# Performance work log

Hardware: AMD Instinct MI355X
Metric: run time of the kernel (lower is better)

The kernel has to match this reference:

```python
import jax, jax.numpy as jnp
import numpy as np

MOE_TOP_K = 2
MOE_GATE_NORM_STD = 1.0  # moe_gate_norm_std


def setup_inputs() -> dict:
    key = jax.random.key(0)
    k1, k2, k3, k4 = jax.random.split(key, 4)
    T, D, E = 16384, 2048, 8
    return {
        "x": jax.random.normal(k1, (T, D), dtype=jnp.float32),
        "wg_weight": jax.random.normal(k2, (E, D), dtype=jnp.float32) * 0.02,
        "gate_map_weight": jax.random.normal(k3, (E, E), dtype=jnp.float32) * 0.1,
        "gate_residual": jax.random.normal(k4, (T, E), dtype=jnp.float32),
    }


def reference(x, wg_weight, gate_map_weight, gate_residual):
    # Router GEMM in fp32 (module force-casts wg and input to float32)
    logits = jnp.einsum("td,ed->te", x.astype(jnp.float32), wg_weight)  # [T, E]
    # gate_residual path: gate_map Linear(E, E, bias=False)
    logits = logits + jnp.einsum("te,fe->tf", gate_residual, gate_map_weight)

    num_experts = wg_weight.shape[0]
    # gating(): moe_use_mixtral_gating=False, moe_use_logits_norm=True
    # torch.std is unbiased (ddof=1)
    logits_std = jnp.std(logits, axis=1, keepdims=True, ddof=1)
    probs = jax.nn.softmax(logits / (logits_std / MOE_GATE_NORM_STD), axis=1)
    gates, indices = jax.lax.top_k(probs, MOE_TOP_K)  # [T, K]
    # zero out routing to the last expert, then renormalize
    gates = jnp.where(indices == num_experts - 1, jnp.zeros_like(gates), gates)
    gates = gates / jnp.sum(gates, axis=1, keepdims=True)
    # Dense equivalent of the per-expert nonzero-gather dict: (indices, gates)
    # fully determines expert_info[e] = (tokens where indices==e, matching gates).
    return gates, indices, logits
```

## Files before the change

### kernel.cpp

```cpp
#include <hip/hip_runtime.h>
#include <hip/hip_bf16.h>
#include <stdint.h>


#define WAVES_PER_BLOCK 4
#define TOKENS_PER_WAVE 8
#define TOKENS_PER_BLOCK (WAVES_PER_BLOCK * TOKENS_PER_WAVE)
#define DCONST 2048
#define NCHUNK 8

__device__ __forceinline__ unsigned long long shfl_xor_u64(unsigned long long v, int m) {
    int lo = __shfl_xor((int)(uint32_t)v, m, 64);
    int hi = __shfl_xor((int)(uint32_t)(v >> 32), m, 64);
    return ((unsigned long long)(uint32_t)hi << 32) | (unsigned long long)(uint32_t)lo;
}

__global__ __launch_bounds__(256, 2)
void router_kernel(const float* __restrict__ x,
                   const float* __restrict__ wg,
                   const float* __restrict__ gm,
                   const float* __restrict__ gr,
                   float* __restrict__ out,
                   int T)
{
    const int wave = threadIdx.x >> 6;
    const int lane = threadIdx.x & 63;
    const int t0   = blockIdx.x * TOKENS_PER_BLOCK + wave * TOKENS_PER_WAVE;

    __shared__ float swg[8 * DCONST];
    {
        const float4* src = (const float4*)wg;
        float4*       dst = (float4*)swg;
        #pragma unroll
        for (int i = 0; i < 16; ++i)
            dst[threadIdx.x + i * 256] = src[threadIdx.x + i * 256];
    }
    __syncthreads();

    float acc[64];
    #pragma unroll
    for (int v = 0; v < 64; ++v) acc[v] = 0.f;

    const float* xw = x + (size_t)t0 * DCONST + (lane << 2);
    const float* wl = swg + (lane << 2);

    float4 xa[8], xb[8];

    #define LOADX(buf, j)                                                     \
        { _Pragma("unroll")                                                   \
          for (int tt = 0; tt < 8; ++tt)                                      \
              buf[tt] = *(const float4*)(xw + tt * DCONST + (j) * 256); }

    #define COMPUTE(j, buf)                                                   \
        { _Pragma("unroll")                                                   \
          for (int e = 0; e < 8; ++e) {                                       \
              const float4 wf = *(const float4*)(wl + e * DCONST + (j) * 256);\
              _Pragma("unroll")                                               \
              for (int tt = 0; tt < 8; ++tt) {                                \
                  acc[tt * 8 + e] += buf[tt].x * wf.x;                        \
                  acc[tt * 8 + e] += buf[tt].y * wf.y;                        \
                  acc[tt * 8 + e] += buf[tt].z * wf.z;                        \
                  acc[tt * 8 + e] += buf[tt].w * wf.w;                        \
              }                                                               \
          } }

    LOADX(xa, 0);
    #pragma unroll 1
    for (int j = 0; j < NCHUNK - 2; j += 2) {
        LOADX(xb, j + 1);
        COMPUTE(j, xa);
        LOADX(xa, j + 2);
        COMPUTE(j + 1, xb);
    }
    LOADX(xb, NCHUNK - 1);
    COMPUTE(NCHUNK - 2, xa);
    COMPUTE(NCHUNK - 1, xb);

    #pragma unroll
    for (int m = 1; m < 64; m <<= 1) {
        const bool up = (lane & m) != 0;
        #pragma unroll
        for (int v = 0; v < 64; v += 2 * m) {
            const float keep = up ? acc[v + m] : acc[v];
            const float send = up ? acc[v] : acc[v + m];
            const float got  = __shfl_xor(send, m, 64);
            acc[v] = keep + got;
        }
    }
    float logit = acc[0];

    const int tt = lane >> 3;
    const int f  = lane & 7;
    const int t  = t0 + tt;

    const float4 ga = *(const float4*)(gr + (size_t)t * 8);
    const float4 gb = *(const float4*)(gr + (size_t)t * 8 + 4);
    const float4 ma = *(const float4*)(gm + f * 8);
    const float4 mb = *(const float4*)(gm + f * 8 + 4);
    logit += ga.x * ma.x + ga.y * ma.y + ga.z * ma.z + ga.w * ma.w
           + gb.x * mb.x + gb.y * mb.y + gb.z * mb.z + gb.w * mb.w;

    out[(size_t)4 * T + (size_t)t0 * 8 + lane] = logit;

    float s = logit;
    s += __shfl_xor(s, 1, 64);
    s += __shfl_xor(s, 2, 64);
    s += __shfl_xor(s, 4, 64);
    const float mean = s * 0.125f;
    float d2 = (logit - mean) * (logit - mean);
    d2 += __shfl_xor(d2, 1, 64);
    d2 += __shfl_xor(d2, 2, 64);
    d2 += __shfl_xor(d2, 4, 64);
    const float stdv = sqrtf(d2 / 7.0f);

    uint32_t ob = __float_as_uint(logit);
    ob = (ob & 0x80000000u) ? ~ob : (ob | 0x80000000u);
    unsigned long long k1 = ((unsigned long long)ob << 8) | (unsigned long long)(7 - f);
    unsigned long long k2 = 0ull;
    #pragma unroll
    for (int m = 1; m <= 4; m <<= 1) {
        const unsigned long long o1 = shfl_xor_u64(k1, m);
        const unsigned long long o2 = shfl_xor_u64(k2, m);
        const unsigned long long hi = k1 > o1 ? k1 : o1;
        const unsigned long long lo = k1 > o1 ? o1 : k1;
        const unsigned long long so = k2 > o2 ? k2 : o2;
        k1 = hi;
        k2 = lo > so ? lo : so;
    }
    const int i1 = 7 - (int)(k1 & 0xFFull);
    const int i2 = 7 - (int)(k2 & 0xFFull);
    uint32_t b1 = (uint32_t)(k1 >> 8), b2 = (uint32_t)(k2 >> 8);
    b1 = (b1 & 0x80000000u) ? (b1 ^ 0x80000000u) : ~b1;
    b2 = (b2 & 0x80000000u) ? (b2 ^ 0x80000000u) : ~b2;
    const float l1 = __uint_as_float(b1);
    const float l2 = __uint_as_float(b2);

    float g0, g1;
    if (i1 == 7)      { g0 = 0.f; g1 = 1.f; }
    else if (i2 == 7) { g0 = 1.f; g1 = 0.f; }
    else {
        const float p = 1.0f / (1.0f + __expf(-(l1 - l2) / stdv));
        g0 = p; g1 = 1.0f - p;
    }

    if (f == 0) out[(size_t)2 * t]             = g0;
    if (f == 1) out[(size_t)2 * t + 1]         = g1;
    if (f == 2) out[(size_t)2 * T + 2 * t]     = (float)i1;
    if (f == 3) out[(size_t)2 * T + 2 * t + 1] = (float)i2;
}

extern "C" void kernel_launch(void* const* d_in, const int* in_sizes, int n_in,
                              void* d_out, int out_size, void* d_ws, size_t ws_size,
                              hipStream_t stream) {
    const float* x  = (const float*)d_in[0];
    const float* wg = (const float*)d_in[1];
    const float* gm = (const float*)d_in[2];
    const float* gr = (const float*)d_in[3];
    const int T = in_sizes[0] / DCONST;
    const int blocks = T / TOKENS_PER_BLOCK;
    router_kernel<<<blocks, 256, 0, stream>>>(x, wg, gm, gr, (float*)d_out, T);
}
```

Measured before the change: 195.4 us.

## Halve tokens per wave and stage router weights in two LDS halves

Each wave now handles 4 tokens instead of 8, which halves the accumulator registers. The 64 KB weight tile in LDS becomes a 32 KB half loaded twice with a barrier between the halves, and launch bounds go up to 4 blocks per CU. The butterfly reduction is shortened, with a final cross-half shuffle, and only the lower 32 lanes write outputs. This targets occupancy and latency hiding for the memory-bound x stream, at the cost of twice as many blocks, each reloading weights, plus extra syncs.

```diff
diff --git a/kernel.cpp b/kernel.cpp
--- a/kernel.cpp
+++ b/kernel.cpp
@@ -3,11 +3,11 @@
 #include <stdint.h>
 
 
+#define TOKENS_PER_WAVE 4
 #define WAVES_PER_BLOCK 4
-#define TOKENS_PER_WAVE 8
-#define TOKENS_PER_BLOCK (WAVES_PER_BLOCK * TOKENS_PER_WAVE)
+#define TOKENS_PER_BLOCK (TOKENS_PER_WAVE * WAVES_PER_BLOCK)
 #define DCONST 2048
-#define NCHUNK 8
+#define HALF_D 1024
 
 __device__ __forceinline__ unsigned long long shfl_xor_u64(unsigned long long v, int m) {
     int lo = __shfl_xor((int)(uint32_t)v, m, 64);
@@ -15,7 +15,7 @@
     return ((unsigned long long)(uint32_t)hi << 32) | (unsigned long long)(uint32_t)lo;
 }
 
-__global__ __launch_bounds__(256, 2)
+__global__ __launch_bounds__(256, 4)
 void router_kernel(const float* __restrict__ x,
                    const float* __restrict__ wg,
                    const float* __restrict__ gm,
@@ -27,36 +27,28 @@
     const int lane = threadIdx.x & 63;
     const int t0   = blockIdx.x * TOKENS_PER_BLOCK + wave * TOKENS_PER_WAVE;
 
-    __shared__ float swg[8 * DCONST];
-    {
-        const float4* src = (const float4*)wg;
-        float4*       dst = (float4*)swg;
-        #pragma unroll
-        for (int i = 0; i < 16; ++i)
-            dst[threadIdx.x + i * 256] = src[threadIdx.x + i * 256];
-    }
-    __syncthreads();
+    __shared__ float swg[8 * HALF_D];
 
-    float acc[64];
+    float acc[32];
     #pragma unroll
-    for (int v = 0; v < 64; ++v) acc[v] = 0.f;
+    for (int v = 0; v < 32; ++v) acc[v] = 0.f;
 
     const float* xw = x + (size_t)t0 * DCONST + (lane << 2);
     const float* wl = swg + (lane << 2);
 
-    float4 xa[8], xb[8];
+    float4 xa[TOKENS_PER_WAVE], xb[TOKENS_PER_WAVE];
 
-    #define LOADX(buf, j)                                                     \
+    #define LOADX(buf, g)                                                     \
         { _Pragma("unroll")                                                   \
-          for (int tt = 0; tt < 8; ++tt)                                      \
-              buf[tt] = *(const float4*)(xw + tt * DCONST + (j) * 256); }
+          for (int tt = 0; tt < TOKENS_PER_WAVE; ++tt)                        \
+              buf[tt] = *(const float4*)(xw + tt * DCONST + (g) * 256); }
 
     #define COMPUTE(j, buf)                                                   \
         { _Pragma("unroll")                                                   \
           for (int e = 0; e < 8; ++e) {                                       \
-              const float4 wf = *(const float4*)(wl + e * DCONST + (j) * 256);\
+              const float4 wf = *(const float4*)(wl + e * HALF_D + (j) * 256);\
               _Pragma("unroll")                                               \
-              for (int tt = 0; tt < 8; ++tt) {                                \
+              for (int tt = 0; tt < TOKENS_PER_WAVE; ++tt) {                  \
                   acc[tt * 8 + e] += buf[tt].x * wf.x;                        \
                   acc[tt * 8 + e] += buf[tt].y * wf.y;                        \
                   acc[tt * 8 + e] += buf[tt].z * wf.z;                        \
@@ -64,33 +56,49 @@
               }                                                               \
           } }
 
-    LOADX(xa, 0);
     #pragma unroll 1
-    for (int j = 0; j < NCHUNK - 2; j += 2) {
-        LOADX(xb, j + 1);
-        COMPUTE(j, xa);
-        LOADX(xa, j + 2);
-        COMPUTE(j + 1, xb);
+    for (int p = 0; p < 2; ++p) {
+        if (p) __syncthreads();
+        {
+            const float4* src = (const float4*)wg;
+            float4*       dst = (float4*)swg;
+            #pragma unroll
+            for (int i = 0; i < 8; ++i) {
+                const int idx = threadIdx.x + i * 256;
+                const int e   = idx >> 8;
+                const int c4  = idx & 255;
+                dst[idx] = src[e * 512 + p * 256 + c4];
+            }
+        }
+        __syncthreads();
+
+        const int g0 = p * 4;
+        LOADX(xa, g0);
+        LOADX(xb, g0 + 1);
+        COMPUTE(0, xa);
+        LOADX(xa, g0 + 2);
+        COMPUTE(1, xb);
+        LOADX(xb, g0 + 3);
+        COMPUTE(2, xa);
+        COMPUTE(3, xb);
     }
-    LOADX(xb, NCHUNK - 1);
-    COMPUTE(NCHUNK - 2, xa);
-    COMPUTE(NCHUNK - 1, xb);
 
     #pragma unroll
-    for (int m = 1; m < 64; m <<= 1) {
+    for (int m = 1; m < 32; m <<= 1) {
         const bool up = (lane & m) != 0;
         #pragma unroll
-        for (int v = 0; v < 64; v += 2 * m) {
+        for (int v = 0; v < 32; v += 2 * m) {
             const float keep = up ? acc[v + m] : acc[v];
             const float send = up ? acc[v] : acc[v + m];
             const float got  = __shfl_xor(send, m, 64);
             acc[v] = keep + got;
         }
     }
-    float logit = acc[0];
+    float logit = acc[0] + __shfl_xor(acc[0], 32, 64);
 
-    const int tt = lane >> 3;
-    const int f  = lane & 7;
+    const int vv = lane & 31;
+    const int tt = vv >> 3;
+    const int f  = vv & 7;
     const int t  = t0 + tt;
 
     const float4 ga = *(const float4*)(gr + (size_t)t * 8);
@@ -100,7 +108,8 @@
     logit += ga.x * ma.x + ga.y * ma.y + ga.z * ma.z + ga.w * ma.w
            + gb.x * mb.x + gb.y * mb.y + gb.z * mb.z + gb.w * mb.w;
 
-    out[(size_t)4 * T + (size_t)t0 * 8 + lane] = logit;
+    if (lane < 32)
+        out[(size_t)4 * T + (size_t)t0 * 8 + lane] = logit;
 
     float s = logit;
     s += __shfl_xor(s, 1, 64);
@@ -143,10 +152,12 @@
         g0 = p; g1 = 1.0f - p;
     }
 
-    if (f == 0) out[(size_t)2 * t]             = g0;
-    if (f == 1) out[(size_t)2 * t + 1]         = g1;
-    if (f == 2) out[(size_t)2 * T + 2 * t]     = (float)i1;
-    if (f == 3) out[(size_t)2 * T + 2 * t + 1] = (float)i2;
+    if (lane < 32) {
+        if (f == 0) out[(size_t)2 * t]             = g0;
+        if (f == 1) out[(size_t)2 * t + 1]         = g1;
+        if (f == 2) out[(size_t)2 * T + 2 * t]     = (float)i1;
+        if (f == 3) out[(size_t)2 * T + 2 * t + 1] = (float)i2;
+    }
 }
 
 extern "C" void kernel_launch(void* const* d_in, const int* in_sizes, int n_in,
```

Result: slower. 225.3 us (+15.3%).

## Split router into split-K GEMM kernel with register-held weights plus epilogue kernel

Applied to the files above, without the earlier changes.

The fused kernel is replaced by two kernels. The first splits the hidden dimension into 8 slices per wave, keeps that slice of the gate weights in registers instead of staging all of them in LDS, and loops over 4 token batches. It writes partial logits to a workspace. A second kernel sums the partials and runs the gating epilogue. The aim is to drop the large LDS footprint and per-block weight copy so occupancy can rise. The cost is a second launch and a workspace round trip.

```diff
diff --git a/kernel.cpp b/kernel.cpp
--- a/kernel.cpp
+++ b/kernel.cpp
@@ -3,11 +3,10 @@
 #include <stdint.h>
 
 
-#define WAVES_PER_BLOCK 4
-#define TOKENS_PER_WAVE 8
-#define TOKENS_PER_BLOCK (WAVES_PER_BLOCK * TOKENS_PER_WAVE)
 #define DCONST 2048
-#define NCHUNK 8
+#define TOK_PER_BATCH 8
+#define BATCHES 4
+#define TOK_PER_WAVE (TOK_PER_BATCH * BATCHES)
 
 __device__ __forceinline__ unsigned long long shfl_xor_u64(unsigned long long v, int m) {
     int lo = __shfl_xor((int)(uint32_t)v, m, 64);
@@ -15,79 +14,94 @@
     return ((unsigned long long)(uint32_t)hi << 32) | (unsigned long long)(uint32_t)lo;
 }
 
-__global__ __launch_bounds__(256, 2)
-void router_kernel(const float* __restrict__ x,
-                   const float* __restrict__ wg,
-                   const float* __restrict__ gm,
-                   const float* __restrict__ gr,
-                   float* __restrict__ out,
-                   int T)
+__global__ __launch_bounds__(256, 3)
+void router_gemm(const float* __restrict__ x,
+                 const float* __restrict__ wg,
+                 float* __restrict__ ws,
+                 int T)
+{
+    const int wave  = threadIdx.x >> 6;
+    const int lane  = threadIdx.x & 63;
+    const int W     = blockIdx.x * 4 + wave;
+    const int g     = W & 7;
+    const int tbase = (W >> 3) * TOK_PER_WAVE;
+
+    const float* wgp = wg + g * 256 + (lane << 2);
+    float4 w8[8];
+    #pragma unroll
+    for (int e = 0; e < 8; ++e)
+        w8[e] = *(const float4*)(wgp + e * DCONST);
+
+    const float* xp = x + (size_t)tbase * DCONST + g * 256 + (lane << 2);
+
+    float4 xa[4], xb[4];
+
+    #define LOADH(buf, trow)                                                  \
+        { _Pragma("unroll")                                                   \
+          for (int i = 0; i < 4; ++i)                                         \
+              buf[i] = *(const float4*)(xp + (size_t)((trow) + i) * DCONST); }
+
+    #define FMAH(buf, tloc0)                                                  \
+        { _Pragma("unroll")                                                   \
+          for (int i = 0; i < 4; ++i) {                                       \
+              _Pragma("unroll")                                               \
+              for (int e = 0; e < 8; ++e) {                                   \
+                  float a = acc[((tloc0) + i) * 8 + e];                       \
+                  a += buf[i].x * w8[e].x;                                    \
+                  a += buf[i].y * w8[e].y;                                    \
+                  a += buf[i].z * w8[e].z;                                    \
+                  a += buf[i].w * w8[e].w;                                    \
+                  acc[((tloc0) + i) * 8 + e] = a;                             \
+              }                                                               \
+          } }
+
+    LOADH(xa, 0);
+    LOADH(xb, 4);
+
+    #pragma unroll 1
+    for (int b = 0; b < BATCHES; ++b) {
+        float acc[64];
+        #pragma unroll
+        for (int v = 0; v < 64; ++v) acc[v] = 0.f;
+
+        FMAH(xa, 0);
+        if (b < BATCHES - 1) LOADH(xa, (b + 1) * 8);
+        FMAH(xb, 4);
+        if (b < BATCHES - 1) LOADH(xb, (b + 1) * 8 + 4);
+
+        #pragma unroll
+        for (int m = 1; m < 64; m <<= 1) {
+            const bool up = (lane & m) != 0;
+            #pragma unroll
+            for (int v = 0; v < 64; v += 2 * m) {
+                const float keep = up ? acc[v + m] : acc[v];
+                const float send = up ? acc[v] : acc[v + m];
+                const float got  = __shfl_xor(send, m, 64);
+                acc[v] = keep + got;
+            }
+        }
+
+        const int tb = (tbase + b * TOK_PER_BATCH) >> 3;
+        ws[(size_t)tb * 512 + g * 64 + lane] = acc[0];
+    }
+}
+
+__global__ __launch_bounds__(256)
+void router_epilogue(const float* __restrict__ ws,
+                     const float* __restrict__ gm,
+                     const float* __restrict__ gr,
+                     float* __restrict__ out,
+                     int T)
 {
     const int wave = threadIdx.x >> 6;
     const int lane = threadIdx.x & 63;
-    const int t0   = blockIdx.x * TOKENS_PER_BLOCK + wave * TOKENS_PER_WAVE;
+    const int tb   = blockIdx.x * 4 + wave;
+    const int t0   = tb * 8;
 
-    __shared__ float swg[8 * DCONST];
-    {
-        const float4* src = (const float4*)wg;
-        float4*       dst = (float4*)swg;
-        #pragma unroll
-        for (int i = 0; i < 16; ++i)
-            dst[threadIdx.x + i * 256] = src[threadIdx.x + i * 256];
-    }
-    __syncthreads();
-
-    float acc[64];
+    float logit = 0.f;
     #pragma unroll
-    for (int v = 0; v < 64; ++v) acc[v] = 0.f;
-
-    const float* xw = x + (size_t)t0 * DCONST + (lane << 2);
-    const float* wl = swg + (lane << 2);
-
-    float4 xa[8], xb[8];
-
-    #define LOADX(buf, j)                                                     \
-        { _Pragma("unroll")                                                   \
-          for (int tt = 0; tt < 8; ++tt)                                      \
-              buf[tt] = *(const float4*)(xw + tt * DCONST + (j) * 256); }
-
-    #define COMPUTE(j, buf)                                                   \
-        { _Pragma("unroll")                                                   \
-          for (int e = 0; e < 8; ++e) {                                       \
-              const float4 wf = *(const float4*)(wl + e * DCONST + (j) * 256);\
-              _Pragma("unroll")                                               \
-              for (int tt = 0; tt < 8; ++tt) {                                \
-                  acc[tt * 8 + e] += buf[tt].x * wf.x;                        \
-                  acc[tt * 8 + e] += buf[tt].y * wf.y;                        \
-                  acc[tt * 8 + e] += buf[tt].z * wf.z;                        \
-                  acc[tt * 8 + e] += buf[tt].w * wf.w;                        \
-              }                                                               \
-          } }
-
-    LOADX(xa, 0);
-    #pragma unroll 1
-    for (int j = 0; j < NCHUNK - 2; j += 2) {
-        LOADX(xb, j + 1);
-        COMPUTE(j, xa);
-        LOADX(xa, j + 2);
-        COMPUTE(j + 1, xb);
-    }
-    LOADX(xb, NCHUNK - 1);
-    COMPUTE(NCHUNK - 2, xa);
-    COMPUTE(NCHUNK - 1, xb);
-
-    #pragma unroll
-    for (int m = 1; m < 64; m <<= 1) {
-        const bool up = (lane & m) != 0;
-        #pragma unroll
-        for (int v = 0; v < 64; v += 2 * m) {
-            const float keep = up ? acc[v + m] : acc[v];
-            const float send = up ? acc[v] : acc[v + m];
-            const float got  = __shfl_xor(send, m, 64);
-            acc[v] = keep + got;
-        }
-    }
-    float logit = acc[0];
+    for (int g = 0; g < 8; ++g)
+        logit += ws[(size_t)tb * 512 + g * 64 + lane];
 
     const int tt = lane >> 3;
     const int f  = lane & 7;
@@ -156,7 +170,12 @@
     const float* wg = (const float*)d_in[1];
     const float* gm = (const float*)d_in[2];
     const float* gr = (const float*)d_in[3];
+    float* ws = (float*)d_ws;
     const int T = in_sizes[0] / DCONST;
-    const int blocks = T / TOKENS_PER_BLOCK;
-    router_kernel<<<blocks, 256, 0, stream>>>(x, wg, gm, gr, (float*)d_out, T);
+
+    const int gemm_blocks = (8 * (T / TOK_PER_WAVE)) / 4;
+    router_gemm<<<gemm_blocks, 256, 0, stream>>>(x, wg, ws, T);
+
+    const int epi_blocks = T / 32;
+    router_epilogue<<<epi_blocks, 256, 0, stream>>>(ws, gm, gr, (float*)d_out, T);
 }
```

After: 199.1 us. No clear change (+1.9%).
